# Kernel tuning notes

Measured on AMD Instinct MI355X. Metric: run time of the kernel, lower is better.

The kernel has to match this reference:

```python
import jax, jax.numpy as jnp
import numpy as np

B, S, H, DFF, E, K = 2, 2048, 1024, 2048, 8, 2


def setup_inputs() -> dict:
    key = jax.random.key(0)
    ks = jax.random.split(key, 8)
    sc_h = 1.0 / np.sqrt(H)
    sc_f = 1.0 / np.sqrt(DFF)
    x = jax.random.normal(ks[0], (B, S, H), dtype=jnp.float32)
    Wg = jax.random.uniform(ks[1], (E, H), jnp.float32, -sc_h, sc_h)  # gate (no bias)
    W1 = jax.random.uniform(ks[2], (E, DFF, H), jnp.float32, -sc_h, sc_h)  # SiGLU gate proj
    b1 = jax.random.uniform(ks[3], (E, DFF), jnp.float32, -sc_h, sc_h)
    W2 = jax.random.uniform(ks[4], (E, DFF, H), jnp.float32, -sc_h, sc_h)  # SiGLU value proj
    b2 = jax.random.uniform(ks[5], (E, DFF), jnp.float32, -sc_h, sc_h)
    W3 = jax.random.uniform(ks[6], (E, H, DFF), jnp.float32, -sc_f, sc_f)  # down proj
    b3 = jax.random.uniform(ks[7], (E, H), jnp.float32, -sc_f, sc_f)
    return {"x": x, "Wg": Wg, "W1": W1, "b1": b1, "W2": W2, "b2": b2, "W3": W3, "b3": b3}


def _moe(x, Wg, W1, b1, W2, b2, W3, b3):
    Bm, Sm, Hm = x.shape
    xt = x.reshape(-1, Hm)  # [T, H]
    gout = xt @ Wg.T  # [T, E]
    topv, topi = jax.lax.top_k(gout, K)  # [T, K]
    w = jax.nn.softmax(topv, axis=-1)  # [T, K]
    # combine weights per expert: comb[t, e] = sum_k w[t,k] * 1[topi[t,k]==e]
    comb = jnp.einsum('tke,tk->te', jax.nn.one_hot(topi, E, dtype=x.dtype), w)  # [T, E]
    # dense per-expert FFN (fixed-shape equivalent of the gather/scatter loop)
    g = jnp.einsum('th,efh->etf', xt, W1) + b1[:, None, :]  # [E, T, DFF]
    v = jnp.einsum('th,efh->etf', xt, W2) + b2[:, None, :]
    h = jax.nn.silu(g) * v  # SiGLU
    eo = jnp.einsum('etf,ehf->eth', h, W3) + b3[:, None, :]  # [E, T, H]
    out = jnp.einsum('eth,te->th', eo, comb)
    return out.reshape(Bm, Sm, Hm)


def reference(x, Wg, W1, b1, W2, b2, W3, b3):
    return _moe(x, Wg, W1, b1, W2, b2, W3, b3)
```

## Files before the change

kernel.cpp:

```cpp
#include <hip/hip_runtime.h>
#include <hip/hip_bf16.h>

#define T_TOK 4096
#define H_DIM 1024
#define DFF_D 2048
#define E_NUM 8
#define K_TOP 2
#define MAXJOBS64 136
#define MAXJOBS128 72

typedef __attribute__((ext_vector_type(8))) short s16x8;
typedef __attribute__((ext_vector_type(4))) float f32x4;

__device__ __forceinline__ ushort f2bf(float f) {
    unsigned u = __float_as_uint(f);
    u = (u + 0x7FFFu + ((u >> 16) & 1u)) >> 16;
    return (ushort)u;
}

__device__ __forceinline__ float bf2f(short s) {
    return __uint_as_float(((unsigned)(ushort)s) << 16);
}

__device__ __forceinline__ void glds16(const ushort* g, ushort* l) {
    __builtin_amdgcn_global_load_lds(
        (const __attribute__((address_space(1))) unsigned*)g,
        (__attribute__((address_space(3))) unsigned*)l, 16, 0, 0);
}

__device__ __forceinline__ s16x8 lds_frag(const ushort* base, int row, int bytecol) {
    int byte = row * 128 + (bytecol ^ ((row & 7) << 4));
    return *(const s16x8*)((const char*)base + byte);
}

__device__ __forceinline__ void cvt8(const float* p, ushort* dst, size_t i) {
    float4 a = ((const float4*)(p + i * 8))[0];
    float4 b = ((const float4*)(p + i * 8))[1];
    union { ushort us[8]; uint4 q; } o;
    o.us[0] = f2bf(a.x); o.us[1] = f2bf(a.y); o.us[2] = f2bf(a.z); o.us[3] = f2bf(a.w);
    o.us[4] = f2bf(b.x); o.us[5] = f2bf(b.y); o.us[6] = f2bf(b.z); o.us[7] = f2bf(b.w);
    ((uint4*)dst)[i] = o.q;
}

__global__ __launch_bounds__(256) void cvt_kernel(
    const float* __restrict__ in, ushort* __restrict__ out, int n8)
{
    int i = blockIdx.x * blockDim.x + threadIdx.x;
    const int stride = gridDim.x * blockDim.x;
    for (; i < n8; i += stride) cvt8(in, out, i);
}

__global__ __launch_bounds__(256) void cvt3_kernel(
    const float* __restrict__ x,  ushort* __restrict__ xbf,
    const float* __restrict__ W1, ushort* __restrict__ w1bf,
    const float* __restrict__ W2, ushort* __restrict__ w2bf)
{
    const int nW = E_NUM * DFF_D * H_DIM / 8;
    const int nX = T_TOK * H_DIM / 8;
    const int total = 2 * nW + nX;
    int i = blockIdx.x * blockDim.x + threadIdx.x;
    const int stride = gridDim.x * blockDim.x;
    for (; i < total; i += stride) {
        if (i < nW)            cvt8(W1, w1bf, i);
        else if (i < 2 * nW)   cvt8(W2, w2bf, i - nW);
        else                   cvt8(x,  xbf,  i - 2 * nW);
    }
}

__global__ __launch_bounds__(256) void gate_kernel(
    const float* __restrict__ x, const float* __restrict__ Wg,
    int* __restrict__ topi_packed, float* __restrict__ wt_slot)
{
    const int t = blockIdx.x * 4 + (threadIdx.x >> 6);
    const int lane = threadIdx.x & 63;
    const float* xr = x + (size_t)t * H_DIM;
    float xv[16];
    #pragma unroll
    for (int j = 0; j < 16; ++j) xv[j] = xr[j * 64 + lane];

    float score[E_NUM];
    #pragma unroll
    for (int e = 0; e < E_NUM; ++e) {
        const float* wr = Wg + e * H_DIM;
        float p = 0.f;
        #pragma unroll
        for (int j = 0; j < 16; ++j) p += xv[j] * wr[j * 64 + lane];
        #pragma unroll
        for (int s = 32; s >= 1; s >>= 1) p += __shfl_xor(p, s, 64);
        score[e] = p;
    }
    if (lane == 0) {
        int i0 = 0;
        #pragma unroll
        for (int e = 1; e < E_NUM; ++e) if (score[e] > score[i0]) i0 = e;
        int i1 = (i0 == 0) ? 1 : 0;
        #pragma unroll
        for (int e = 0; e < E_NUM; ++e)
            if (e != i0 && score[e] > score[i1]) i1 = e;
        float e1 = expf(score[i1] - score[i0]);
        float w0 = 1.f / (1.f + e1);
        float w1 = e1 / (1.f + e1);
        topi_packed[t] = i0 | (i1 << 8);
        wt_slot[t * K_TOP + 0] = w0;
        wt_slot[t * K_TOP + 1] = w1;
    }
}

__global__ __launch_bounds__(256) void build_lists(
    const int* __restrict__ topi_packed,
    int* __restrict__ cnt, int* __restrict__ tok_list, int* __restrict__ slot_list)
{
    const int e = blockIdx.x;
    __shared__ int lcnt;
    if (threadIdx.x == 0) lcnt = 0;
    __syncthreads();
    for (int t = threadIdx.x; t < T_TOK; t += 256) {
        int pk = topi_packed[t];
        int i0 = pk & 0xff;
        int i1 = (pk >> 8) & 0xff;
        if (i0 == e) {
            int p = atomicAdd(&lcnt, 1);
            tok_list[e * T_TOK + p] = t;
            slot_list[e * T_TOK + p] = t * K_TOP + 0;
        }
        if (i1 == e) {
            int p = atomicAdd(&lcnt, 1);
            tok_list[e * T_TOK + p] = t;
            slot_list[e * T_TOK + p] = t * K_TOP + 1;
        }
    }
    __syncthreads();
    if (threadIdx.x == 0) cnt[e] = lcnt;
}

__global__ void build_jobs(const int* __restrict__ cnt,
                           int* __restrict__ jobs64, int* __restrict__ jobs128,
                           int* __restrict__ njobs)
{
    if (threadIdx.x == 0 && blockIdx.x == 0) {
        int n = 0, n2 = 0;
        for (int e = 0; e < E_NUM; ++e) {
            int mt = (cnt[e] + 63) >> 6;
            for (int m = 0; m < mt; ++m) jobs64[n++] = (e << 16) | m;
            int mt2 = (cnt[e] + 127) >> 7;
            for (int m = 0; m < mt2; ++m) jobs128[n2++] = (e << 16) | m;
        }
        njobs[0] = n;
        njobs[1] = n2;
    }
}

__global__ __launch_bounds__(256) void up_kernel(
    const ushort* __restrict__ xbf,
    const ushort* __restrict__ w1bf, const float* __restrict__ b1,
    const ushort* __restrict__ w2bf, const float* __restrict__ b2,
    const int* __restrict__ cnt, const int* __restrict__ tok_list,
    const int* __restrict__ slot_list, const float* __restrict__ wt_slot,
    const int* __restrict__ jobs128, const int* __restrict__ njobs,
    ushort* __restrict__ h)
{
    if ((int)blockIdx.y >= njobs[1]) return;
    const int jb = jobs128[blockIdx.y];
    const int e = jb >> 16;
    const int mbase = (jb & 0xffff) * 128;
    const int M = cnt[e];
    const int nbase = blockIdx.x * 64;
    const int tid = threadIdx.x;
    const int lane = tid & 63;
    const int w = tid >> 6;

    __shared__ ushort As[128 * 64];
    __shared__ ushort B1s[64 * 64];
    __shared__ ushort B2s[64 * 64];

    const ushort* srcA[4];
    const ushort* srcB1[2];
    const ushort* srcB2[2];
    #pragma unroll
    for (int j = 0; j < 4; ++j) {
        int o = j * 4096 + tid * 16;
        int r = o >> 7;
        int cb = (o & 127) ^ ((r & 7) << 4);
        int lpos = mbase + r; if (lpos > M - 1) lpos = M - 1;
        int tok = tok_list[e * T_TOK + lpos];
        srcA[j] = xbf + (size_t)tok * H_DIM + (cb >> 1);
    }
    #pragma unroll
    for (int j = 0; j < 2; ++j) {
        int o = j * 4096 + tid * 16;
        int r = o >> 7;
        int cb = (o & 127) ^ ((r & 7) << 4);
        srcB1[j] = w1bf + ((size_t)e * DFF_D + nbase + r) * H_DIM + (cb >> 1);
        srcB2[j] = w2bf + ((size_t)e * DFF_D + nbase + r) * H_DIM + (cb >> 1);
    }

    const f32x4 zero = {0.f, 0.f, 0.f, 0.f};
    f32x4 accg[2][4], accv[2][4];
    #pragma unroll
    for (int mi = 0; mi < 2; ++mi)
        #pragma unroll
        for (int ni = 0; ni < 4; ++ni) { accg[mi][ni] = zero; accv[mi][ni] = zero; }

    const int r16 = lane & 15;
    const int g4  = lane >> 4;
    const int cb0 = g4 * 16;

    for (int k0 = 0; k0 < H_DIM; k0 += 64) {
        #pragma unroll
        for (int j = 0; j < 4; ++j)
            glds16(srcA[j] + k0, &As[j * 2048 + (tid >> 3) * 64 + (tid & 7) * 8]);
        #pragma unroll
        for (int j = 0; j < 2; ++j) {
            glds16(srcB1[j] + k0, &B1s[j * 2048 + (tid >> 3) * 64 + (tid & 7) * 8]);
            glds16(srcB2[j] + k0, &B2s[j * 2048 + (tid >> 3) * 64 + (tid & 7) * 8]);
        }
        __syncthreads();
        #pragma unroll
        for (int kk = 0; kk < 2; ++kk) {
            s16x8 bf1[4], bf2[4];
            #pragma unroll
            for (int ni = 0; ni < 4; ++ni) {
                bf1[ni] = lds_frag(B1s, ni * 16 + r16, kk * 64 + cb0);
                bf2[ni] = lds_frag(B2s, ni * 16 + r16, kk * 64 + cb0);
            }
            #pragma unroll
            for (int mi = 0; mi < 2; ++mi) {
                s16x8 af = lds_frag(As, w * 32 + mi * 16 + r16, kk * 64 + cb0);
                #pragma unroll
                for (int ni = 0; ni < 4; ++ni) {
                    accg[mi][ni] = __builtin_amdgcn_mfma_f32_16x16x32_bf16(af, bf1[ni], accg[mi][ni], 0, 0, 0);
                    accv[mi][ni] = __builtin_amdgcn_mfma_f32_16x16x32_bf16(af, bf2[ni], accv[mi][ni], 0, 0, 0);
                }
            }
        }
        __syncthreads();
    }

    #pragma unroll
    for (int mi = 0; mi < 2; ++mi) {
        #pragma unroll
        for (int j = 0; j < 4; ++j) {
            int p = mbase + w * 32 + mi * 16 + g4 * 4 + j;
            if (p < M) {
                int slot = slot_list[e * T_TOK + p];
                float wgt = wt_slot[slot];
                #pragma unroll
                for (int ni = 0; ni < 4; ++ni) {
                    int col = nbase + ni * 16 + r16;
                    float g = accg[mi][ni][j] + b1[e * DFF_D + col];
                    float v = accv[mi][ni][j] + b2[e * DFF_D + col];
                    float s = g / (1.f + __expf(-g));
                    h[(size_t)slot * DFF_D + col] = f2bf(wgt * s * v);
                }
            }
        }
    }
}

__global__ __launch_bounds__(256) void down_kernel(
    const ushort* __restrict__ h,
    const ushort* __restrict__ w3bf,
    const int* __restrict__ cnt, const int* __restrict__ slot_list,
    const int* __restrict__ jobs64, const int* __restrict__ njobs,
    ushort* __restrict__ eo)
{
    if ((int)blockIdx.y >= njobs[0]) return;
    const int jb = jobs64[blockIdx.y];
    const int e = jb >> 16;
    const int mbase = (jb & 0xffff) * 64;
    const int M = cnt[e];
    const int nbase = blockIdx.x * 128;
    const int tid = threadIdx.x;
    const int lane = tid & 63;
    const int w = tid >> 6;

    __shared__ ushort As[64 * 64];
    __shared__ ushort Bs[128 * 64];

    const ushort* srcA[2];
    const ushort* srcB[4];
    #pragma unroll
    for (int j = 0; j < 2; ++j) {
        int o = j * 4096 + tid * 16;
        int r = o >> 7;
        int cb = (o & 127) ^ ((r & 7) << 4);
        int lpos = mbase + r; if (lpos > M - 1) lpos = M - 1;
        int slot = slot_list[e * T_TOK + lpos];
        srcA[j] = h + (size_t)slot * DFF_D + (cb >> 1);
    }
    #pragma unroll
    for (int j = 0; j < 4; ++j) {
        int o = j * 4096 + tid * 16;
        int r = o >> 7;
        int cb = (o & 127) ^ ((r & 7) << 4);
        srcB[j] = w3bf + ((size_t)e * H_DIM + nbase + r) * DFF_D + (cb >> 1);
    }

    const f32x4 zero = {0.f, 0.f, 0.f, 0.f};
    f32x4 acc[8];
    #pragma unroll
    for (int ni = 0; ni < 8; ++ni) acc[ni] = zero;

    const int r16 = lane & 15;
    const int g4  = lane >> 4;
    const int cb0 = g4 * 16;

    for (int k0 = 0; k0 < DFF_D; k0 += 64) {
        #pragma unroll
        for (int j = 0; j < 2; ++j)
            glds16(srcA[j] + k0, &As[j * 2048 + (tid >> 3) * 64 + (tid & 7) * 8]);
        #pragma unroll
        for (int j = 0; j < 4; ++j)
            glds16(srcB[j] + k0, &Bs[j * 2048 + (tid >> 3) * 64 + (tid & 7) * 8]);
        __syncthreads();
        #pragma unroll
        for (int kk = 0; kk < 2; ++kk) {
            s16x8 af = lds_frag(As, w * 16 + r16, kk * 64 + cb0);
            #pragma unroll
            for (int ni = 0; ni < 8; ++ni) {
                s16x8 bf = lds_frag(Bs, ni * 16 + r16, kk * 64 + cb0);
                acc[ni] = __builtin_amdgcn_mfma_f32_16x16x32_bf16(af, bf, acc[ni], 0, 0, 0);
            }
        }
        __syncthreads();
    }

    #pragma unroll
    for (int j = 0; j < 4; ++j) {
        int p = mbase + w * 16 + g4 * 4 + j;
        if (p < M) {
            int slot = slot_list[e * T_TOK + p];
            #pragma unroll
            for (int ni = 0; ni < 8; ++ni) {
                int col = nbase + ni * 16 + r16;
                eo[(size_t)slot * H_DIM + col] = f2bf(acc[ni][j]);
            }
        }
    }
}

__global__ __launch_bounds__(256) void combine_kernel(
    const ushort* __restrict__ eo, const int* __restrict__ topi_packed,
    const float* __restrict__ wt_slot, const float* __restrict__ b3,
    float* __restrict__ out)
{
    const int i = blockIdx.x * 256 + threadIdx.x;
    const int t = i >> 7;
    const int c0 = (i & 127) * 8;
    const int pk = topi_packed[t];
    const int e0 = pk & 0xff, e1 = (pk >> 8) & 0xff;
    const float w0 = wt_slot[2 * t], w1 = wt_slot[2 * t + 1];
    s16x8 a = *(const s16x8*)(eo + (size_t)(2 * t) * H_DIM + c0);
    s16x8 b = *(const s16x8*)(eo + (size_t)(2 * t + 1) * H_DIM + c0);
    const float4* p0 = (const float4*)(b3 + e0 * H_DIM + c0);
    const float4* p1 = (const float4*)(b3 + e1 * H_DIM + c0);
    float4 b0a = p0[0], b0b = p0[1];
    float4 b1a = p1[0], b1b = p1[1];
    float4 r0, r1;
    r0.x = bf2f(a[0]) + bf2f(b[0]) + w0 * b0a.x + w1 * b1a.x;
    r0.y = bf2f(a[1]) + bf2f(b[1]) + w0 * b0a.y + w1 * b1a.y;
    r0.z = bf2f(a[2]) + bf2f(b[2]) + w0 * b0a.z + w1 * b1a.z;
    r0.w = bf2f(a[3]) + bf2f(b[3]) + w0 * b0a.w + w1 * b1a.w;
    r1.x = bf2f(a[4]) + bf2f(b[4]) + w0 * b0b.x + w1 * b1b.x;
    r1.y = bf2f(a[5]) + bf2f(b[5]) + w0 * b0b.y + w1 * b1b.y;
    r1.z = bf2f(a[6]) + bf2f(b[6]) + w0 * b0b.z + w1 * b1b.z;
    r1.w = bf2f(a[7]) + bf2f(b[7]) + w0 * b0b.w + w1 * b1b.w;
    float4* op = (float4*)(out + (size_t)t * H_DIM + c0);
    op[0] = r0;
    op[1] = r1;
}

extern "C" void kernel_launch(void* const* d_in, const int* in_sizes, int n_in,
                              void* d_out, int out_size, void* d_ws, size_t ws_size,
                              hipStream_t stream) {
    const float* x  = (const float*)d_in[0];
    const float* Wg = (const float*)d_in[1];
    const float* W1 = (const float*)d_in[2];
    const float* b1 = (const float*)d_in[3];
    const float* W2 = (const float*)d_in[4];
    const float* b2 = (const float*)d_in[5];
    const float* W3 = (const float*)d_in[6];
    const float* b3 = (const float*)d_in[7];
    float* out = (float*)d_out;

    char* ws = (char*)d_ws;
    int*   cnt       = (int*)(ws);
    int*   njobs     = (int*)(ws + 64);
    int*   jobs64    = (int*)(ws + 128);
    int*   jobs128   = (int*)(ws + 704);
    int*   tok_list  = (int*)(ws + 1024);
    int*   slot_list = (int*)(ws + 1024 + E_NUM * T_TOK * 4);
    float* wt_slot   = (float*)(ws + 1024 + 2 * E_NUM * T_TOK * 4);
    int*   topi      = (int*)(ws + 320 * 1024);
    ushort* xbf  = (ushort*)(ws + (size_t)1  * (1u << 20));
    ushort* w1bf = (ushort*)(ws + (size_t)16 * (1u << 20));
    ushort* w2bf = (ushort*)(ws + (size_t)48 * (1u << 20));
    ushort* hbuf = (ushort*)(ws + (size_t)80 * (1u << 20));
    ushort* w3bf = w2bf;
    ushort* eobf = w1bf;

    cvt3_kernel<<<2048, 256, 0, stream>>>(x, xbf, W1, w1bf, W2, w2bf);

    gate_kernel<<<T_TOK / 4, 256, 0, stream>>>(x, Wg, topi, wt_slot);
    build_lists<<<E_NUM, 256, 0, stream>>>(topi, cnt, tok_list, slot_list);
    build_jobs<<<1, 64, 0, stream>>>(cnt, jobs64, jobs128, njobs);

    dim3 gup(DFF_D / 64, MAXJOBS128);
    up_kernel<<<gup, 256, 0, stream>>>(xbf, w1bf, b1, w2bf, b2, cnt, tok_list,
                                       slot_list, wt_slot, jobs128, njobs, hbuf);

    cvt_kernel<<<2048, 256, 0, stream>>>(W3, w3bf, E_NUM * H_DIM * DFF_D / 8);

    dim3 gdn(H_DIM / 128, MAXJOBS64);
    down_kernel<<<gdn, 256, 0, stream>>>(hbuf, w3bf, cnt, slot_list,
                                         jobs64, njobs, eobf);

    combine_kernel<<<T_TOK * H_DIM / 8 / 256, 256, 0, stream>>>(eobf, topi, wt_slot, b3, out);
}
```

Baseline: 260.4 us.

## Interleave W1/W2 into one bf16 matrix and use 128x128 tiles in up/down GEMMs

The bf16 conversion now interleaves W1 and W2 rows in 16-row groups into a single combined weight matrix. This lets the up-projection kernel run a single 128x128 GEMM tile per block with a 2x2 wave layout, where each wave's gate and value accumulators for the same column sit in adjacent fragments. The down-projection kernel moves from 64x128 to 128x128 tiles with the same 2x2 wave layout, so both kernels share one 128-row job list. Larger tiles raise data reuse per LDS load and halve the number of down-kernel blocks, at the cost of more accumulator registers and more padding waste for expert counts that are not multiples of 128.

```diff
diff --git a/kernel.cpp b/kernel.cpp
--- a/kernel.cpp
+++ b/kernel.cpp
@@ -6,8 +6,7 @@
 #define DFF_D 2048
 #define E_NUM 8
 #define K_TOP 2
-#define MAXJOBS64 136
-#define MAXJOBS128 72
+#define MAXJOBS 72
 
 typedef __attribute__((ext_vector_type(8))) short s16x8;
 typedef __attribute__((ext_vector_type(4))) float f32x4;
@@ -33,13 +32,13 @@
     return *(const s16x8*)((const char*)base + byte);
 }
 
-__device__ __forceinline__ void cvt8(const float* p, ushort* dst, size_t i) {
-    float4 a = ((const float4*)(p + i * 8))[0];
-    float4 b = ((const float4*)(p + i * 8))[1];
+__device__ __forceinline__ void cvt8p(const float* src, ushort* dst) {
+    float4 a = ((const float4*)src)[0];
+    float4 b = ((const float4*)src)[1];
     union { ushort us[8]; uint4 q; } o;
     o.us[0] = f2bf(a.x); o.us[1] = f2bf(a.y); o.us[2] = f2bf(a.z); o.us[3] = f2bf(a.w);
     o.us[4] = f2bf(b.x); o.us[5] = f2bf(b.y); o.us[6] = f2bf(b.z); o.us[7] = f2bf(b.w);
-    ((uint4*)dst)[i] = o.q;
+    *(uint4*)dst = o.q;
 }
 
 __global__ __launch_bounds__(256) void cvt_kernel(
@@ -47,23 +46,32 @@
 {
     int i = blockIdx.x * blockDim.x + threadIdx.x;
     const int stride = gridDim.x * blockDim.x;
-    for (; i < n8; i += stride) cvt8(in, out, i);
+    for (; i < n8; i += stride) cvt8p(in + (size_t)i * 8, out + (size_t)i * 8);
 }
 
 __global__ __launch_bounds__(256) void cvt3_kernel(
     const float* __restrict__ x,  ushort* __restrict__ xbf,
-    const float* __restrict__ W1, ushort* __restrict__ w1bf,
-    const float* __restrict__ W2, ushort* __restrict__ w2bf)
-{
-    const int nW = E_NUM * DFF_D * H_DIM / 8;
+    const float* __restrict__ W1, const float* __restrict__ W2,
+    ushort* __restrict__ w12bf)
+{
+    const int nW12 = E_NUM * 2 * DFF_D * H_DIM / 8;
     const int nX = T_TOK * H_DIM / 8;
-    const int total = 2 * nW + nX;
     int i = blockIdx.x * blockDim.x + threadIdx.x;
     const int stride = gridDim.x * blockDim.x;
-    for (; i < total; i += stride) {
-        if (i < nW)            cvt8(W1, w1bf, i);
-        else if (i < 2 * nW)   cvt8(W2, w2bf, i - nW);
-        else                   cvt8(x,  xbf,  i - 2 * nW);
+    for (; i < nW12 + nX; i += stride) {
+        if (i < nW12) {
+            int r = i >> 7;
+            int c8 = i & 127;
+            int e = r >> 12;
+            int vr = r & 4095;
+            int mat = (vr >> 4) & 1;
+            int srow = ((vr >> 5) << 4) | (vr & 15);
+            const float* src = (mat ? W2 : W1) + ((size_t)e * DFF_D + srow) * H_DIM + c8 * 8;
+            cvt8p(src, w12bf + (size_t)i * 8);
+        } else {
+            int j = i - nW12;
+            cvt8p(x + (size_t)j * 8, xbf + (size_t)j * 8);
+        }
     }
 }
 
@@ -134,48 +142,42 @@
 }
 
 __global__ void build_jobs(const int* __restrict__ cnt,
-                           int* __restrict__ jobs64, int* __restrict__ jobs128,
-                           int* __restrict__ njobs)
+                           int* __restrict__ jobs, int* __restrict__ njobs)
 {
     if (threadIdx.x == 0 && blockIdx.x == 0) {
-        int n = 0, n2 = 0;
+        int n = 0;
         for (int e = 0; e < E_NUM; ++e) {
-            int mt = (cnt[e] + 63) >> 6;
-            for (int m = 0; m < mt; ++m) jobs64[n++] = (e << 16) | m;
-            int mt2 = (cnt[e] + 127) >> 7;
-            for (int m = 0; m < mt2; ++m) jobs128[n2++] = (e << 16) | m;
+            int mt = (cnt[e] + 127) >> 7;
+            for (int m = 0; m < mt; ++m) jobs[n++] = (e << 16) | m;
         }
         njobs[0] = n;
-        njobs[1] = n2;
     }
 }
 
 __global__ __launch_bounds__(256) void up_kernel(
-    const ushort* __restrict__ xbf,
-    const ushort* __restrict__ w1bf, const float* __restrict__ b1,
-    const ushort* __restrict__ w2bf, const float* __restrict__ b2,
+    const ushort* __restrict__ xbf, const ushort* __restrict__ w12bf,
+    const float* __restrict__ b1, const float* __restrict__ b2,
     const int* __restrict__ cnt, const int* __restrict__ tok_list,
     const int* __restrict__ slot_list, const float* __restrict__ wt_slot,
-    const int* __restrict__ jobs128, const int* __restrict__ njobs,
+    const int* __restrict__ jobs, const int* __restrict__ njobs,
     ushort* __restrict__ h)
 {
-    if ((int)blockIdx.y >= njobs[1]) return;
-    const int jb = jobs128[blockIdx.y];
+    if ((int)blockIdx.y >= njobs[0]) return;
+    const int jb = jobs[blockIdx.y];
     const int e = jb >> 16;
     const int mbase = (jb & 0xffff) * 128;
     const int M = cnt[e];
-    const int nbase = blockIdx.x * 64;
+    const int nvbase = blockIdx.x * 128;
     const int tid = threadIdx.x;
     const int lane = tid & 63;
     const int w = tid >> 6;
+    const int wr = w >> 1, wc = w & 1;
 
     __shared__ ushort As[128 * 64];
-    __shared__ ushort B1s[64 * 64];
-    __shared__ ushort B2s[64 * 64];
+    __shared__ ushort Bs[128 * 64];
 
     const ushort* srcA[4];
-    const ushort* srcB1[2];
-    const ushort* srcB2[2];
+    const ushort* srcB[4];
     #pragma unroll
     for (int j = 0; j < 4; ++j) {
         int o = j * 4096 + tid * 16;
@@ -184,22 +186,15 @@
         int lpos = mbase + r; if (lpos > M - 1) lpos = M - 1;
         int tok = tok_list[e * T_TOK + lpos];
         srcA[j] = xbf + (size_t)tok * H_DIM + (cb >> 1);
-    }
-    #pragma unroll
-    for (int j = 0; j < 2; ++j) {
-        int o = j * 4096 + tid * 16;
-        int r = o >> 7;
-        int cb = (o & 127) ^ ((r & 7) << 4);
-        srcB1[j] = w1bf + ((size_t)e * DFF_D + nbase + r) * H_DIM + (cb >> 1);
-        srcB2[j] = w2bf + ((size_t)e * DFF_D + nbase + r) * H_DIM + (cb >> 1);
+        srcB[j] = w12bf + ((size_t)e * 2 * DFF_D + nvbase + r) * H_DIM + (cb >> 1);
     }
 
     const f32x4 zero = {0.f, 0.f, 0.f, 0.f};
-    f32x4 accg[2][4], accv[2][4];
-    #pragma unroll
-    for (int mi = 0; mi < 2; ++mi)
-        #pragma unroll
-        for (int ni = 0; ni < 4; ++ni) { accg[mi][ni] = zero; accv[mi][ni] = zero; }
+    f32x4 acc[4][4];
+    #pragma unroll
+    for (int mi = 0; mi < 4; ++mi)
+        #pragma unroll
+        for (int ni = 0; ni < 4; ++ni) acc[mi][ni] = zero;
 
     const int r16 = lane & 15;
     const int g4  = lane >> 4;
@@ -207,48 +202,41 @@
 
     for (int k0 = 0; k0 < H_DIM; k0 += 64) {
         #pragma unroll
-        for (int j = 0; j < 4; ++j)
-            glds16(srcA[j] + k0, &As[j * 2048 + (tid >> 3) * 64 + (tid & 7) * 8]);
-        #pragma unroll
-        for (int j = 0; j < 2; ++j) {
-            glds16(srcB1[j] + k0, &B1s[j * 2048 + (tid >> 3) * 64 + (tid & 7) * 8]);
-            glds16(srcB2[j] + k0, &B2s[j * 2048 + (tid >> 3) * 64 + (tid & 7) * 8]);
+        for (int j = 0; j < 4; ++j) {
+            glds16(srcA[j] + k0, &As[j * 2048 + tid * 8]);
+            glds16(srcB[j] + k0, &Bs[j * 2048 + tid * 8]);
         }
         __syncthreads();
         #pragma unroll
         for (int kk = 0; kk < 2; ++kk) {
-            s16x8 bf1[4], bf2[4];
+            s16x8 bf[4];
             #pragma unroll
-            for (int ni = 0; ni < 4; ++ni) {
-                bf1[ni] = lds_frag(B1s, ni * 16 + r16, kk * 64 + cb0);
-                bf2[ni] = lds_frag(B2s, ni * 16 + r16, kk * 64 + cb0);
+            for (int ni = 0; ni < 4; ++ni)
+                bf[ni] = lds_frag(Bs, wc * 64 + ni * 16 + r16, kk * 64 + cb0);
+            #pragma unroll
+            for (int mi = 0; mi < 4; ++mi) {
+                s16x8 af = lds_frag(As, wr * 64 + mi * 16 + r16, kk * 64 + cb0);
+                #pragma unroll
+                for (int ni = 0; ni < 4; ++ni)
+                    acc[mi][ni] = __builtin_amdgcn_mfma_f32_16x16x32_bf16(af, bf[ni], acc[mi][ni], 0, 0, 0);
             }
-            #pragma unroll
-            for (int mi = 0; mi < 2; ++mi) {
-                s16x8 af = lds_frag(As, w * 32 + mi * 16 + r16, kk * 64 + cb0);
-                #pragma unroll
-                for (int ni = 0; ni < 4; ++ni) {
-                    accg[mi][ni] = __builtin_amdgcn_mfma_f32_16x16x32_bf16(af, bf1[ni], accg[mi][ni], 0, 0, 0);
-                    accv[mi][ni] = __builtin_amdgcn_mfma_f32_16x16x32_bf16(af, bf2[ni], accv[mi][ni], 0, 0, 0);
-                }
-            }
         }
         __syncthreads();
     }
 
     #pragma unroll
-    for (int mi = 0; mi < 2; ++mi) {
+    for (int mi = 0; mi < 4; ++mi) {
         #pragma unroll
         for (int j = 0; j < 4; ++j) {
-            int p = mbase + w * 32 + mi * 16 + g4 * 4 + j;
+            int p = mbase + wr * 64 + mi * 16 + g4 * 4 + j;
             if (p < M) {
                 int slot = slot_list[e * T_TOK + p];
                 float wgt = wt_slot[slot];
                 #pragma unroll
-                for (int ni = 0; ni < 4; ++ni) {
-                    int col = nbase + ni * 16 + r16;
-                    float g = accg[mi][ni][j] + b1[e * DFF_D + col];
-                    float v = accv[mi][ni][j] + b2[e * DFF_D + col];
+                for (int q = 0; q < 2; ++q) {
+                    int col = blockIdx.x * 64 + wc * 32 + q * 16 + r16;
+                    float g = acc[mi][2 * q][j]     + b1[e * DFF_D + col];
+                    float v = acc[mi][2 * q + 1][j] + b2[e * DFF_D + col];
                     float s = g / (1.f + __expf(-g));
                     h[(size_t)slot * DFF_D + col] = f2bf(wgt * s * v);
                 }
@@ -261,45 +249,42 @@
     const ushort* __restrict__ h,
     const ushort* __restrict__ w3bf,
     const int* __restrict__ cnt, const int* __restrict__ slot_list,
-    const int* __restrict__ jobs64, const int* __restrict__ njobs,
+    const int* __restrict__ jobs, const int* __restrict__ njobs,
     ushort* __restrict__ eo)
 {
     if ((int)blockIdx.y >= njobs[0]) return;
-    const int jb = jobs64[blockIdx.y];
+    const int jb = jobs[blockIdx.y];
     const int e = jb >> 16;
-    const int mbase = (jb & 0xffff) * 64;
+    const int mbase = (jb & 0xffff) * 128;
     const int M = cnt[e];
     const int nbase = blockIdx.x * 128;
     const int tid = threadIdx.x;
     const int lane = tid & 63;
     const int w = tid >> 6;
-
-    __shared__ ushort As[64 * 64];
+    const int wr = w >> 1, wc = w & 1;
+
+    __shared__ ushort As[128 * 64];
     __shared__ ushort Bs[128 * 64];
 
-    const ushort* srcA[2];
+    const ushort* srcA[4];
     const ushort* srcB[4];
     #pragma unroll
-    for (int j = 0; j < 2; ++j) {
+    for (int j = 0; j < 4; ++j) {
         int o = j * 4096 + tid * 16;
         int r = o >> 7;
         int cb = (o & 127) ^ ((r & 7) << 4);
         int lpos = mbase + r; if (lpos > M - 1) lpos = M - 1;
         int slot = slot_list[e * T_TOK + lpos];
         srcA[j] = h + (size_t)slot * DFF_D + (cb >> 1);
-    }
-    #pragma unroll
-    for (int j = 0; j < 4; ++j) {
-        int o = j * 4096 + tid * 16;
-        int r = o >> 7;
-        int cb = (o & 127) ^ ((r & 7) << 4);
         srcB[j] = w3bf + ((size_t)e * H_DIM + nbase + r) * DFF_D + (cb >> 1);
     }
 
     const f32x4 zero = {0.f, 0.f, 0.f, 0.f};
-    f32x4 acc[8];
-    #pragma unroll
-    for (int ni = 0; ni < 8; ++ni) acc[ni] = zero;
+    f32x4 acc[4][4];
+    #pragma unroll
+    for (int mi = 0; mi < 4; ++mi)
+        #pragma unroll
+        for (int ni = 0; ni < 4; ++ni) acc[mi][ni] = zero;
 
     const int r16 = lane & 15;
     const int g4  = lane >> 4;
@@ -307,33 +292,40 @@
 
     for (int k0 = 0; k0 < DFF_D; k0 += 64) {
         #pragma unroll
-        for (int j = 0; j < 2; ++j)
-            glds16(srcA[j] + k0, &As[j * 2048 + (tid >> 3) * 64 + (tid & 7) * 8]);
-        #pragma unroll
-        for (int j = 0; j < 4; ++j)
-            glds16(srcB[j] + k0, &Bs[j * 2048 + (tid >> 3) * 64 + (tid & 7) * 8]);
+        for (int j = 0; j < 4; ++j) {
+            glds16(srcA[j] + k0, &As[j * 2048 + tid * 8]);
+            glds16(srcB[j] + k0, &Bs[j * 2048 + tid * 8]);
+        }
         __syncthreads();
         #pragma unroll
         for (int kk = 0; kk < 2; ++kk) {
-            s16x8 af = lds_frag(As, w * 16 + r16, kk * 64 + cb0);
+            s16x8 bf[4];
             #pragma unroll
-            for (int ni = 0; ni < 8; ++ni) {
-                s16x8 bf = lds_frag(Bs, ni * 16 + r16, kk * 64 + cb0);
-                acc[ni] = __builtin_amdgcn_mfma_f32_16x16x32_bf16(af, bf, acc[ni], 0, 0, 0);
+            for (int ni = 0; ni < 4; ++ni)
+                bf[ni] = lds_frag(Bs, wc * 64 + ni * 16 + r16, kk * 64 + cb0);
+            #pragma unroll
+            for (int mi = 0; mi < 4; ++mi) {
+                s16x8 af = lds_frag(As, wr * 64 + mi * 16 + r16, kk * 64 + cb0);
+                #pragma unroll
+                for (int ni = 0; ni < 4; ++ni)
+                    acc[mi][ni] = __builtin_amdgcn_mfma_f32_16x16x32_bf16(af, bf[ni], acc[mi][ni], 0, 0, 0);
             }
         }
         __syncthreads();
     }
 
     #pragma unroll
-    for (int j = 0; j < 4; ++j) {
-        int p = mbase + w * 16 + g4 * 4 + j;
-        if (p < M) {
-            int slot = slot_list[e * T_TOK + p];
-            #pragma unroll
-            for (int ni = 0; ni < 8; ++ni) {
-                int col = nbase + ni * 16 + r16;
-                eo[(size_t)slot * H_DIM + col] = f2bf(acc[ni][j]);
+    for (int mi = 0; mi < 4; ++mi) {
+        #pragma unroll
+        for (int j = 0; j < 4; ++j) {
+            int p = mbase + wr * 64 + mi * 16 + g4 * 4 + j;
+            if (p < M) {
+                int slot = slot_list[e * T_TOK + p];
+                #pragma unroll
+                for (int ni = 0; ni < 4; ++ni) {
+                    int col = nbase + wc * 64 + ni * 16 + r16;
+                    eo[(size_t)slot * H_DIM + col] = f2bf(acc[mi][ni][j]);
+                }
             }
         }
     }
@@ -386,34 +378,32 @@
     char* ws = (char*)d_ws;
     int*   cnt       = (int*)(ws);
     int*   njobs     = (int*)(ws + 64);
-    int*   jobs64    = (int*)(ws + 128);
-    int*   jobs128   = (int*)(ws + 704);
+    int*   jobs      = (int*)(ws + 128);
     int*   tok_list  = (int*)(ws + 1024);
     int*   slot_list = (int*)(ws + 1024 + E_NUM * T_TOK * 4);
     float* wt_slot   = (float*)(ws + 1024 + 2 * E_NUM * T_TOK * 4);
     int*   topi      = (int*)(ws + 320 * 1024);
-    ushort* xbf  = (ushort*)(ws + (size_t)1  * (1u << 20));
-    ushort* w1bf = (ushort*)(ws + (size_t)16 * (1u << 20));
-    ushort* w2bf = (ushort*)(ws + (size_t)48 * (1u << 20));
-    ushort* hbuf = (ushort*)(ws + (size_t)80 * (1u << 20));
-    ushort* w3bf = w2bf;
-    ushort* eobf = w1bf;
-
-    cvt3_kernel<<<2048, 256, 0, stream>>>(x, xbf, W1, w1bf, W2, w2bf);
+    ushort* xbf   = (ushort*)(ws + (size_t)1  * (1u << 20));
+    ushort* w12bf = (ushort*)(ws + (size_t)16 * (1u << 20));
+    ushort* hbuf  = (ushort*)(ws + (size_t)80 * (1u << 20));
+    ushort* w3bf  = (ushort*)(ws + (size_t)16 * (1u << 20));
+    ushort* eobf  = (ushort*)(ws + (size_t)48 * (1u << 20));
+
+    cvt3_kernel<<<2048, 256, 0, stream>>>(x, xbf, W1, W2, w12bf);
 
     gate_kernel<<<T_TOK / 4, 256, 0, stream>>>(x, Wg, topi, wt_slot);
     build_lists<<<E_NUM, 256, 0, stream>>>(topi, cnt, tok_list, slot_list);
-    build_jobs<<<1, 64, 0, stream>>>(cnt, jobs64, jobs128, njobs);
-
-    dim3 gup(DFF_D / 64, MAXJOBS128);
-    up_kernel<<<gup, 256, 0, stream>>>(xbf, w1bf, b1, w2bf, b2, cnt, tok_list,
-                                       slot_list, wt_slot, jobs128, njobs, hbuf);
+    build_jobs<<<1, 64, 0, stream>>>(cnt, jobs, njobs);
+
+    dim3 gup(2 * DFF_D / 128, MAXJOBS);
+    up_kernel<<<gup, 256, 0, stream>>>(xbf, w12bf, b1, b2, cnt, tok_list,
+                                       slot_list, wt_slot, jobs, njobs, hbuf);
 
     cvt_kernel<<<2048, 256, 0, stream>>>(W3, w3bf, E_NUM * H_DIM * DFF_D / 8);
 
-    dim3 gdn(H_DIM / 128, MAXJOBS64);
+    dim3 gdn(H_DIM / 128, MAXJOBS);
     down_kernel<<<gdn, 256, 0, stream>>>(hbuf, w3bf, cnt, slot_list,
-                                         jobs64, njobs, eobf);
+                                         jobs, njobs, eobf);
 
     combine_kernel<<<T_TOK * H_DIM / 8 / 256, 256, 0, stream>>>(eobf, topi, wt_slot, b3, out);
 }
```

Result: slower. 288.8 us (+10.9%).

## Fuse fp32-to-bf16 weight conversion into the expert GEMM tile staging

Applied to the files above, without the earlier changes.

Removes the standalone conversion kernels for W1, W2, W3 and x. The up and down GEMMs now read fp32 weights directly, convert them in registers and write swizzled bf16 into LDS; x is converted inside the gate kernel. The down kernel's warp tiling also changes from 4x1 to 2x2. This drops the large write and re-read of the converted weight copies, but weights are now reloaded in fp32 once per token tile. Staging also moves from async global_load_lds to synchronous register loads, which may expose more memory latency.

```diff
diff --git a/kernel.cpp b/kernel.cpp
--- a/kernel.cpp
+++ b/kernel.cpp
@@ -33,43 +33,26 @@
     return *(const s16x8*)((const char*)base + byte);
 }
 
-__device__ __forceinline__ void cvt8(const float* p, ushort* dst, size_t i) {
-    float4 a = ((const float4*)(p + i * 8))[0];
-    float4 b = ((const float4*)(p + i * 8))[1];
-    union { ushort us[8]; uint4 q; } o;
-    o.us[0] = f2bf(a.x); o.us[1] = f2bf(a.y); o.us[2] = f2bf(a.z); o.us[3] = f2bf(a.w);
-    o.us[4] = f2bf(b.x); o.us[5] = f2bf(b.y); o.us[6] = f2bf(b.z); o.us[7] = f2bf(b.w);
-    ((uint4*)dst)[i] = o.q;
-}
-
-__global__ __launch_bounds__(256) void cvt_kernel(
-    const float* __restrict__ in, ushort* __restrict__ out, int n8)
-{
-    int i = blockIdx.x * blockDim.x + threadIdx.x;
-    const int stride = gridDim.x * blockDim.x;
-    for (; i < n8; i += stride) cvt8(in, out, i);
-}
-
-__global__ __launch_bounds__(256) void cvt3_kernel(
-    const float* __restrict__ x,  ushort* __restrict__ xbf,
-    const float* __restrict__ W1, ushort* __restrict__ w1bf,
-    const float* __restrict__ W2, ushort* __restrict__ w2bf)
-{
-    const int nW = E_NUM * DFF_D * H_DIM / 8;
-    const int nX = T_TOK * H_DIM / 8;
-    const int total = 2 * nW + nX;
-    int i = blockIdx.x * blockDim.x + threadIdx.x;
-    const int stride = gridDim.x * blockDim.x;
-    for (; i < total; i += stride) {
-        if (i < nW)            cvt8(W1, w1bf, i);
-        else if (i < 2 * nW)   cvt8(W2, w2bf, i - nW);
-        else                   cvt8(x,  xbf,  i - 2 * nW);
+__device__ __forceinline__ void stage_b32(const float* src, ushort* ldsbase, int row, int kh) {
+    float4 f[8];
+    #pragma unroll
+    for (int j = 0; j < 8; ++j) f[j] = ((const float4*)src)[j];
+    char* lb = (char*)ldsbase + row * 128;
+    const int swz = (row & 7) << 4;
+    #pragma unroll
+    for (int i = 0; i < 4; ++i) {
+        union { ushort us[8]; uint4 q; } o;
+        float4 a = f[2 * i], b = f[2 * i + 1];
+        o.us[0] = f2bf(a.x); o.us[1] = f2bf(a.y); o.us[2] = f2bf(a.z); o.us[3] = f2bf(a.w);
+        o.us[4] = f2bf(b.x); o.us[5] = f2bf(b.y); o.us[6] = f2bf(b.z); o.us[7] = f2bf(b.w);
+        *(uint4*)(lb + ((kh * 64 + i * 16) ^ swz)) = o.q;
     }
 }
 
 __global__ __launch_bounds__(256) void gate_kernel(
     const float* __restrict__ x, const float* __restrict__ Wg,
-    int* __restrict__ topi_packed, float* __restrict__ wt_slot)
+    int* __restrict__ topi_packed, float* __restrict__ wt_slot,
+    ushort* __restrict__ xbf)
 {
     const int t = blockIdx.x * 4 + (threadIdx.x >> 6);
     const int lane = threadIdx.x & 63;
@@ -77,6 +60,10 @@
     float xv[16];
     #pragma unroll
     for (int j = 0; j < 16; ++j) xv[j] = xr[j * 64 + lane];
+
+    ushort* xo = xbf + (size_t)t * H_DIM;
+    #pragma unroll
+    for (int j = 0; j < 16; ++j) xo[j * 64 + lane] = f2bf(xv[j]);
 
     float score[E_NUM];
     #pragma unroll
@@ -152,8 +139,8 @@
 
 __global__ __launch_bounds__(256) void up_kernel(
     const ushort* __restrict__ xbf,
-    const ushort* __restrict__ w1bf, const float* __restrict__ b1,
-    const ushort* __restrict__ w2bf, const float* __restrict__ b2,
+    const float* __restrict__ W1, const float* __restrict__ b1,
+    const float* __restrict__ W2, const float* __restrict__ b2,
     const int* __restrict__ cnt, const int* __restrict__ tok_list,
     const int* __restrict__ slot_list, const float* __restrict__ wt_slot,
     const int* __restrict__ jobs128, const int* __restrict__ njobs,
@@ -174,8 +161,6 @@
     __shared__ ushort B2s[64 * 64];
 
     const ushort* srcA[4];
-    const ushort* srcB1[2];
-    const ushort* srcB2[2];
     #pragma unroll
     for (int j = 0; j < 4; ++j) {
         int o = j * 4096 + tid * 16;
@@ -185,14 +170,13 @@
         int tok = tok_list[e * T_TOK + lpos];
         srcA[j] = xbf + (size_t)tok * H_DIM + (cb >> 1);
     }
-    #pragma unroll
-    for (int j = 0; j < 2; ++j) {
-        int o = j * 4096 + tid * 16;
-        int r = o >> 7;
-        int cb = (o & 127) ^ ((r & 7) << 4);
-        srcB1[j] = w1bf + ((size_t)e * DFF_D + nbase + r) * H_DIM + (cb >> 1);
-        srcB2[j] = w2bf + ((size_t)e * DFF_D + nbase + r) * H_DIM + (cb >> 1);
-    }
+
+    const int u = tid & 127;
+    const int brow = u >> 1;
+    const int bkh = u & 1;
+    const float* srcB = ((tid < 128) ? W1 : W2)
+        + ((size_t)e * DFF_D + nbase + brow) * H_DIM + bkh * 32;
+    ushort* dstB = (tid < 128) ? B1s : B2s;
 
     const f32x4 zero = {0.f, 0.f, 0.f, 0.f};
     f32x4 accg[2][4], accv[2][4];
@@ -208,12 +192,8 @@
     for (int k0 = 0; k0 < H_DIM; k0 += 64) {
         #pragma unroll
         for (int j = 0; j < 4; ++j)
-            glds16(srcA[j] + k0, &As[j * 2048 + (tid >> 3) * 64 + (tid & 7) * 8]);
-        #pragma unroll
-        for (int j = 0; j < 2; ++j) {
-            glds16(srcB1[j] + k0, &B1s[j * 2048 + (tid >> 3) * 64 + (tid & 7) * 8]);
-            glds16(srcB2[j] + k0, &B2s[j * 2048 + (tid >> 3) * 64 + (tid & 7) * 8]);
-        }
+            glds16(srcA[j] + k0, &As[j * 2048 + tid * 8]);
+        stage_b32(srcB + k0, dstB, brow, bkh);
         __syncthreads();
         #pragma unroll
         for (int kk = 0; kk < 2; ++kk) {
@@ -259,7 +239,7 @@
 
 __global__ __launch_bounds__(256) void down_kernel(
     const ushort* __restrict__ h,
-    const ushort* __restrict__ w3bf,
+    const float* __restrict__ W3,
     const int* __restrict__ cnt, const int* __restrict__ slot_list,
     const int* __restrict__ jobs64, const int* __restrict__ njobs,
     ushort* __restrict__ eo)
@@ -273,12 +253,12 @@
     const int tid = threadIdx.x;
     const int lane = tid & 63;
     const int w = tid >> 6;
+    const int wr = w >> 1, wc = w & 1;
 
     __shared__ ushort As[64 * 64];
     __shared__ ushort Bs[128 * 64];
 
     const ushort* srcA[2];
-    const ushort* srcB[4];
     #pragma unroll
     for (int j = 0; j < 2; ++j) {
         int o = j * 4096 + tid * 16;
@@ -288,18 +268,17 @@
         int slot = slot_list[e * T_TOK + lpos];
         srcA[j] = h + (size_t)slot * DFF_D + (cb >> 1);
     }
-    #pragma unroll
-    for (int j = 0; j < 4; ++j) {
-        int o = j * 4096 + tid * 16;
-        int r = o >> 7;
-        int cb = (o & 127) ^ ((r & 7) << 4);
-        srcB[j] = w3bf + ((size_t)e * H_DIM + nbase + r) * DFF_D + (cb >> 1);
-    }
+
+    const int brow = tid >> 1;
+    const int bkh = tid & 1;
+    const float* srcB = W3 + ((size_t)e * H_DIM + nbase + brow) * DFF_D + bkh * 32;
 
     const f32x4 zero = {0.f, 0.f, 0.f, 0.f};
-    f32x4 acc[8];
-    #pragma unroll
-    for (int ni = 0; ni < 8; ++ni) acc[ni] = zero;
+    f32x4 acc[2][4];
+    #pragma unroll
+    for (int mi = 0; mi < 2; ++mi)
+        #pragma unroll
+        for (int ni = 0; ni < 4; ++ni) acc[mi][ni] = zero;
 
     const int r16 = lane & 15;
     const int g4  = lane >> 4;
@@ -308,32 +287,38 @@
     for (int k0 = 0; k0 < DFF_D; k0 += 64) {
         #pragma unroll
         for (int j = 0; j < 2; ++j)
-            glds16(srcA[j] + k0, &As[j * 2048 + (tid >> 3) * 64 + (tid & 7) * 8]);
-        #pragma unroll
-        for (int j = 0; j < 4; ++j)
-            glds16(srcB[j] + k0, &Bs[j * 2048 + (tid >> 3) * 64 + (tid & 7) * 8]);
+            glds16(srcA[j] + k0, &As[j * 2048 + tid * 8]);
+        stage_b32(srcB + k0, Bs, brow, bkh);
         __syncthreads();
         #pragma unroll
         for (int kk = 0; kk < 2; ++kk) {
-            s16x8 af = lds_frag(As, w * 16 + r16, kk * 64 + cb0);
+            s16x8 bf[4];
             #pragma unroll
-            for (int ni = 0; ni < 8; ++ni) {
-                s16x8 bf = lds_frag(Bs, ni * 16 + r16, kk * 64 + cb0);
-                acc[ni] = __builtin_amdgcn_mfma_f32_16x16x32_bf16(af, bf, acc[ni], 0, 0, 0);
+            for (int ni = 0; ni < 4; ++ni)
+                bf[ni] = lds_frag(Bs, wc * 64 + ni * 16 + r16, kk * 64 + cb0);
+            #pragma unroll
+            for (int mi = 0; mi < 2; ++mi) {
+                s16x8 af = lds_frag(As, wr * 32 + mi * 16 + r16, kk * 64 + cb0);
+                #pragma unroll
+                for (int ni = 0; ni < 4; ++ni)
+                    acc[mi][ni] = __builtin_amdgcn_mfma_f32_16x16x32_bf16(af, bf[ni], acc[mi][ni], 0, 0, 0);
             }
         }
         __syncthreads();
     }
 
     #pragma unroll
-    for (int j = 0; j < 4; ++j) {
-        int p = mbase + w * 16 + g4 * 4 + j;
-        if (p < M) {
-            int slot = slot_list[e * T_TOK + p];
-            #pragma unroll
-            for (int ni = 0; ni < 8; ++ni) {
-                int col = nbase + ni * 16 + r16;
-                eo[(size_t)slot * H_DIM + col] = f2bf(acc[ni][j]);
+    for (int mi = 0; mi < 2; ++mi) {
+        #pragma unroll
+        for (int j = 0; j < 4; ++j) {
+            int p = mbase + wr * 32 + mi * 16 + g4 * 4 + j;
+            if (p < M) {
+                int slot = slot_list[e * T_TOK + p];
+                #pragma unroll
+                for (int ni = 0; ni < 4; ++ni) {
+                    int col = nbase + wc * 64 + ni * 16 + r16;
+                    eo[(size_t)slot * H_DIM + col] = f2bf(acc[mi][ni][j]);
+                }
             }
         }
     }
@@ -393,26 +378,19 @@
     float* wt_slot   = (float*)(ws + 1024 + 2 * E_NUM * T_TOK * 4);
     int*   topi      = (int*)(ws + 320 * 1024);
     ushort* xbf  = (ushort*)(ws + (size_t)1  * (1u << 20));
-    ushort* w1bf = (ushort*)(ws + (size_t)16 * (1u << 20));
-    ushort* w2bf = (ushort*)(ws + (size_t)48 * (1u << 20));
-    ushort* hbuf = (ushort*)(ws + (size_t)80 * (1u << 20));
-    ushort* w3bf = w2bf;
-    ushort* eobf = w1bf;
-
-    cvt3_kernel<<<2048, 256, 0, stream>>>(x, xbf, W1, w1bf, W2, w2bf);
-
-    gate_kernel<<<T_TOK / 4, 256, 0, stream>>>(x, Wg, topi, wt_slot);
+    ushort* hbuf = (ushort*)(ws + (size_t)16 * (1u << 20));
+    ushort* eobf = (ushort*)(ws + (size_t)48 * (1u << 20));
+
+    gate_kernel<<<T_TOK / 4, 256, 0, stream>>>(x, Wg, topi, wt_slot, xbf);
     build_lists<<<E_NUM, 256, 0, stream>>>(topi, cnt, tok_list, slot_list);
     build_jobs<<<1, 64, 0, stream>>>(cnt, jobs64, jobs128, njobs);
 
     dim3 gup(DFF_D / 64, MAXJOBS128);
-    up_kernel<<<gup, 256, 0, stream>>>(xbf, w1bf, b1, w2bf, b2, cnt, tok_list,
+    up_kernel<<<gup, 256, 0, stream>>>(xbf, W1, b1, W2, b2, cnt, tok_list,
                                        slot_list, wt_slot, jobs128, njobs, hbuf);
 
-    cvt_kernel<<<2048, 256, 0, stream>>>(W3, w3bf, E_NUM * H_DIM * DFF_D / 8);
-
     dim3 gdn(H_DIM / 128, MAXJOBS64);
-    down_kernel<<<gdn, 256, 0, stream>>>(hbuf, w3bf, cnt, slot_list,
+    down_kernel<<<gdn, 256, 0, stream>>>(hbuf, W3, cnt, slot_list,
                                          jobs64, njobs, eobf);
 
     combine_kernel<<<T_TOK * H_DIM / 8 / 256, 256, 0, stream>>>(eobf, topi, wt_slot, b3, out);
```

Result: slower. 431.7 us (+65.8%).

## Retile down-projection to 128x64 tiles with two waves, simplify LDS store indexing

Applied to the files above, without the earlier changes.

The down kernel moves from 64-row by 128-column tiles with four waves to 128-row by 64-column tiles with two waves. Each wave now computes a 64x64 block of output, which raises MFMA work per fragment load and reuses the B fragments across four M sub-tiles. The grid now uses the 128-row job list. LDS destination addressing in the up kernel is simplified to tid*8, which is equivalent for 256 threads. The trade-off is fewer threads per block, more accumulator registers and more padding waste when an expert's token count is not a multiple of 128.

```diff
diff --git a/kernel.cpp b/kernel.cpp
--- a/kernel.cpp
+++ b/kernel.cpp
@@ -208,11 +208,11 @@
     for (int k0 = 0; k0 < H_DIM; k0 += 64) {
         #pragma unroll
         for (int j = 0; j < 4; ++j)
-            glds16(srcA[j] + k0, &As[j * 2048 + (tid >> 3) * 64 + (tid & 7) * 8]);
+            glds16(srcA[j] + k0, &As[j * 2048 + tid * 8]);
         #pragma unroll
         for (int j = 0; j < 2; ++j) {
-            glds16(srcB1[j] + k0, &B1s[j * 2048 + (tid >> 3) * 64 + (tid & 7) * 8]);
-            glds16(srcB2[j] + k0, &B2s[j * 2048 + (tid >> 3) * 64 + (tid & 7) * 8]);
+            glds16(srcB1[j] + k0, &B1s[j * 2048 + tid * 8]);
+            glds16(srcB2[j] + k0, &B2s[j * 2048 + tid * 8]);
         }
         __syncthreads();
         #pragma unroll
@@ -257,49 +257,51 @@
     }
 }
 
-__global__ __launch_bounds__(256) void down_kernel(
+__global__ __launch_bounds__(128) void down_kernel(
     const ushort* __restrict__ h,
     const ushort* __restrict__ w3bf,
     const int* __restrict__ cnt, const int* __restrict__ slot_list,
-    const int* __restrict__ jobs64, const int* __restrict__ njobs,
+    const int* __restrict__ jobs128, const int* __restrict__ njobs,
     ushort* __restrict__ eo)
 {
-    if ((int)blockIdx.y >= njobs[0]) return;
-    const int jb = jobs64[blockIdx.y];
+    if ((int)blockIdx.y >= njobs[1]) return;
+    const int jb = jobs128[blockIdx.y];
     const int e = jb >> 16;
-    const int mbase = (jb & 0xffff) * 64;
+    const int mbase = (jb & 0xffff) * 128;
     const int M = cnt[e];
-    const int nbase = blockIdx.x * 128;
+    const int nbase = blockIdx.x * 64;
     const int tid = threadIdx.x;
     const int lane = tid & 63;
     const int w = tid >> 6;
 
-    __shared__ ushort As[64 * 64];
-    __shared__ ushort Bs[128 * 64];
-
-    const ushort* srcA[2];
-    const ushort* srcB[4];
-    #pragma unroll
-    for (int j = 0; j < 2; ++j) {
-        int o = j * 4096 + tid * 16;
+    __shared__ ushort As[128 * 64];
+    __shared__ ushort Bs[64 * 64];
+
+    const ushort* srcA[8];
+    #pragma unroll
+    for (int j = 0; j < 8; ++j) {
+        int o = j * 2048 + tid * 16;
         int r = o >> 7;
         int cb = (o & 127) ^ ((r & 7) << 4);
         int lpos = mbase + r; if (lpos > M - 1) lpos = M - 1;
         int slot = slot_list[e * T_TOK + lpos];
         srcA[j] = h + (size_t)slot * DFF_D + (cb >> 1);
     }
+    const ushort* srcB[4];
     #pragma unroll
     for (int j = 0; j < 4; ++j) {
-        int o = j * 4096 + tid * 16;
+        int o = j * 2048 + tid * 16;
         int r = o >> 7;
         int cb = (o & 127) ^ ((r & 7) << 4);
         srcB[j] = w3bf + ((size_t)e * H_DIM + nbase + r) * DFF_D + (cb >> 1);
     }
 
     const f32x4 zero = {0.f, 0.f, 0.f, 0.f};
-    f32x4 acc[8];
-    #pragma unroll
-    for (int ni = 0; ni < 8; ++ni) acc[ni] = zero;
+    f32x4 acc[4][4];
+    #pragma unroll
+    for (int mi = 0; mi < 4; ++mi)
+        #pragma unroll
+        for (int ni = 0; ni < 4; ++ni) acc[mi][ni] = zero;
 
     const int r16 = lane & 15;
     const int g4  = lane >> 4;
@@ -307,33 +309,41 @@
 
     for (int k0 = 0; k0 < DFF_D; k0 += 64) {
         #pragma unroll
-        for (int j = 0; j < 2; ++j)
-            glds16(srcA[j] + k0, &As[j * 2048 + (tid >> 3) * 64 + (tid & 7) * 8]);
+        for (int j = 0; j < 8; ++j)
+            glds16(srcA[j] + k0, &As[j * 1024 + tid * 8]);
         #pragma unroll
         for (int j = 0; j < 4; ++j)
-            glds16(srcB[j] + k0, &Bs[j * 2048 + (tid >> 3) * 64 + (tid & 7) * 8]);
+            glds16(srcB[j] + k0, &Bs[j * 1024 + tid * 8]);
         __syncthreads();
         #pragma unroll
         for (int kk = 0; kk < 2; ++kk) {
-            s16x8 af = lds_frag(As, w * 16 + r16, kk * 64 + cb0);
+            s16x8 bf[4];
             #pragma unroll
-            for (int ni = 0; ni < 8; ++ni) {
-                s16x8 bf = lds_frag(Bs, ni * 16 + r16, kk * 64 + cb0);
-                acc[ni] = __builtin_amdgcn_mfma_f32_16x16x32_bf16(af, bf, acc[ni], 0, 0, 0);
+            for (int ni = 0; ni < 4; ++ni)
+                bf[ni] = lds_frag(Bs, ni * 16 + r16, kk * 64 + cb0);
+            #pragma unroll
+            for (int mi = 0; mi < 4; ++mi) {
+                s16x8 af = lds_frag(As, w * 64 + mi * 16 + r16, kk * 64 + cb0);
+                #pragma unroll
+                for (int ni = 0; ni < 4; ++ni)
+                    acc[mi][ni] = __builtin_amdgcn_mfma_f32_16x16x32_bf16(af, bf[ni], acc[mi][ni], 0, 0, 0);
             }
         }
         __syncthreads();
     }
 
     #pragma unroll
-    for (int j = 0; j < 4; ++j) {
-        int p = mbase + w * 16 + g4 * 4 + j;
-        if (p < M) {
-            int slot = slot_list[e * T_TOK + p];
-            #pragma unroll
-            for (int ni = 0; ni < 8; ++ni) {
-                int col = nbase + ni * 16 + r16;
-                eo[(size_t)slot * H_DIM + col] = f2bf(acc[ni][j]);
+    for (int mi = 0; mi < 4; ++mi) {
+        #pragma unroll
+        for (int j = 0; j < 4; ++j) {
+            int p = mbase + w * 64 + mi * 16 + g4 * 4 + j;
+            if (p < M) {
+                int slot = slot_list[e * T_TOK + p];
+                #pragma unroll
+                for (int ni = 0; ni < 4; ++ni) {
+                    int col = nbase + ni * 16 + r16;
+                    eo[(size_t)slot * H_DIM + col] = f2bf(acc[mi][ni][j]);
+                }
             }
         }
     }
@@ -411,9 +421,9 @@
 
     cvt_kernel<<<2048, 256, 0, stream>>>(W3, w3bf, E_NUM * H_DIM * DFF_D / 8);
 
-    dim3 gdn(H_DIM / 128, MAXJOBS64);
-    down_kernel<<<gdn, 256, 0, stream>>>(hbuf, w3bf, cnt, slot_list,
-                                         jobs64, njobs, eobf);
+    dim3 gdn(H_DIM / 64, MAXJOBS128);
+    down_kernel<<<gdn, 128, 0, stream>>>(hbuf, w3bf, cnt, slot_list,
+                                         jobs128, njobs, eobf);
 
     combine_kernel<<<T_TOK * H_DIM / 8 / 256, 256, 0, stream>>>(eobf, topi, wt_slot, b3, out);
 }
```

After: 260.3 us. About the same (-0.0%).
